# Kernel optimization log

Measured on AMD Instinct MI355X. Metric: run time of the kernel, lower is better.

Reference implementation:

```python
import jax, jax.numpy as jnp
import numpy as np


def setup_inputs() -> dict:
    key = jax.random.key(0)
    ks = jax.random.split(key, 8)
    B, IN, P, D1, D2, C = 1024, 4096, 512, 8, 16, 4
    H1, H2 = D1 * P, D2 * P
    H3 = H2 // 4
    return {
        "data_omics": jax.random.normal(ks[0], (B, IN), jnp.float32),
        "comp": jax.random.randint(ks[1], (IN, P), 0, 2, jnp.int32),
        "fc1_w": jax.random.normal(ks[2], (IN, H1), jnp.float32) * (2.0 / (IN + H1)) ** 0.5,
        "fc1_b": jax.random.uniform(ks[3], (H1,), jnp.float32),
        "fc2_w": jax.random.normal(ks[4], (H1, H2), jnp.float32) * (2.0 / (H1 + H2)) ** 0.5,
        "fc2_b": jax.random.uniform(ks[5], (H2,), jnp.float32),
        "w3": jax.random.normal(ks[6], (H2, H3), jnp.float32) * (2.0 / (H2 + H3)) ** 0.5,
        "b3": jnp.zeros((H3,), jnp.float32),
        "w4": jax.random.normal(ks[7], (H3, C), jnp.float32) * (2.0 / (H3 + C)) ** 0.5,
        "b4": jnp.zeros((C,), jnp.float32),
    }


def reference(data_omics, comp, fc1_w, fc1_b, fc2_w, fc2_b, w3, b3, w4, b4):
    P = comp.shape[1]
    D1 = fc1_w.shape[1] // P          # dim_per_path_1
    D2 = fc2_w.shape[1] // P          # dim_per_path_2
    # mask_1: [input_dim, D1*P] gene->pathway membership, repeated per hidden unit
    mask_1 = jnp.repeat(comp.astype(fc1_w.dtype), D1, axis=1)
    # mask_2: block-diagonal [D1*P, D2*P] with D1xD2 blocks of ones
    mask_2 = jnp.kron(jnp.eye(P, dtype=fc2_w.dtype), jnp.ones((D1, D2), fc2_w.dtype))
    out = jnp.matmul(data_omics, fc1_w * mask_1) + fc1_b      # [B, D1*P]
    out = jnp.matmul(out, fc2_w * mask_2) + fc2_b             # [B, D2*P]
    h = jax.nn.relu(jnp.matmul(out, w3) + b3)                 # dropout is eval no-op
    logits = jnp.matmul(h, w4) + b4                           # [B, num_classes]
    return logits
```

## Files before the change

kernel.cpp:

```cpp
#include <hip/hip_runtime.h>
#include <hip/hip_bf16.h>
#include <cstdint>
#include <cstddef>

typedef __bf16 bf16_t;
typedef __bf16 bf16x8 __attribute__((ext_vector_type(8)));
typedef float f32x4 __attribute__((ext_vector_type(4)));

#define AS1(p) ((const __attribute__((address_space(1))) void*)(p))
#define AS3(p) ((__attribute__((address_space(3))) void*)(p))

struct bf16x4_s { bf16_t x, y, z, w; };

__global__ __launch_bounds__(256) void k_transpose(const float* __restrict__ W,
                                                   const int* __restrict__ comp,
                                                   bf16_t* __restrict__ Bt,
                                                   int K, int N, int Pc) {
  __shared__ float tile[64][65];
  const int k0 = blockIdx.x * 64;
  const int n0 = blockIdx.y * 64;
  const int t = threadIdx.x;
  const int c = t & 63;
  const int r0 = t >> 6;
#pragma unroll
  for (int i = 0; i < 16; ++i) {
    int r = r0 + i * 4;
    float v = W[(size_t)(k0 + r) * N + n0 + c];
    v *= (float)comp[(size_t)(k0 + r) * Pc + ((n0 + c) >> 3)];
    tile[r][c] = v;
  }
  __syncthreads();
#pragma unroll
  for (int i = 0; i < 16; ++i) {
    int r = r0 + i * 4;
    Bt[(size_t)(n0 + r) * K + k0 + c] = (bf16_t)tile[c][r];
  }
}

__global__ __launch_bounds__(256) void k_w23(const float* __restrict__ fc2w,
                                             const float* __restrict__ w3,
                                             const float* __restrict__ b2,
                                             bf16_t* __restrict__ W23t,
                                             float* __restrict__ b23) {
  __shared__ float w3s[128][65];
  const int n0 = blockIdx.x * 64;
  const int pb = blockIdx.y * 8;
  const int tid = threadIdx.x;
  const int c = tid & 63, q = tid >> 6;
#pragma unroll
  for (int i = 0; i < 32; ++i) {
    int rr = i * 4 + q;
    w3s[rr][c] = w3[(size_t)(pb * 16 + rr) * 2048 + n0 + c];
  }
  __syncthreads();
  const int pp = c >> 3;
  const int k1 = pb * 8 + c;
  const int p = pb + pp;
  float f2[16];
  const float4* frp = (const float4*)(fc2w + (size_t)k1 * 8192 + (size_t)p * 16);
#pragma unroll
  for (int t4 = 0; t4 < 4; ++t4) {
    float4 v = frp[t4];
    f2[t4 * 4 + 0] = v.x; f2[t4 * 4 + 1] = v.y; f2[t4 * 4 + 2] = v.z; f2[t4 * 4 + 3] = v.w;
  }
#pragma unroll
  for (int i = 0; i < 16; ++i) {
    int nn = i * 4 + q;
    float s = 0.f;
#pragma unroll
    for (int d2 = 0; d2 < 16; ++d2) {
      int d2r = (d2 + 2 * pp) & 15;
      s += f2[d2r] * w3s[pp * 16 + d2r][nn];
    }
    W23t[(size_t)(n0 + nn) * 4096 + k1] = (bf16_t)s;
  }
  float bp = 0.f;
  for (int rr = q * 32; rr < q * 32 + 32; ++rr)
    bp += b2[pb * 16 + rr] * w3s[rr][c];
  atomicAdd(&b23[n0 + c], bp);
}

template<int MI, int NI, bool AF32>
__global__ __launch_bounds__(256, 2) void k_gemm_sk(const void* __restrict__ Av,
                                                    const bf16_t* __restrict__ Bt,
                                                    float* __restrict__ P,
                                                    int M, int N, int K, int ksub) {
  constexpr int BM = MI * 32;
  constexpr int BN = NI * 32;
  constexpr int BK = 32;
  __shared__ bf16_t As[BM][BK];
  __shared__ bf16_t Bs[BN][BK];
  const int tid = threadIdx.x;
  const int wave = tid >> 6;
  const int lane = tid & 63;
  const int m0 = blockIdx.y * BM;
  const int n0 = blockIdx.x * BN;
  const int kbase = blockIdx.z * ksub;
  const int wm = (wave >> 1) * (MI * 16);
  const int wn = (wave & 1) * (NI * 16);
  const int lrow = lane >> 2;
  const int lk = (lane & 3) * 8;
  const int fr = lane & 15;
  const int fkb = (lane >> 4) * 8;

  f32x4 acc[MI][NI] = {};
  const int nkt = ksub / BK;
  for (int kt = 0; kt < nkt; ++kt) {
    const int k0 = kbase + kt * BK;
    if constexpr (AF32) {
      const float* Af = (const float*)Av;
      for (int i = wave; i < BM / 16; i += 4) {
        const float* g = Af + (size_t)(m0 + i * 16 + lrow) * K + k0 + lk;
        float4 a0 = *(const float4*)g;
        float4 a1 = *(const float4*)(g + 4);
        bf16x8 v;
        v[0] = (bf16_t)a0.x; v[1] = (bf16_t)a0.y; v[2] = (bf16_t)a0.z; v[3] = (bf16_t)a0.w;
        v[4] = (bf16_t)a1.x; v[5] = (bf16_t)a1.y; v[6] = (bf16_t)a1.z; v[7] = (bf16_t)a1.w;
        *reinterpret_cast<bf16x8*>(&As[i * 16 + lrow][lk]) = v;
      }
    } else {
      const bf16_t* Ab = (const bf16_t*)Av;
      for (int i = wave; i < BM / 16; i += 4) {
        const bf16_t* g = Ab + (size_t)(m0 + i * 16 + lrow) * K + k0 + lk;
        __builtin_amdgcn_global_load_lds(AS1(g), AS3(&As[i * 16][0]), 16, 0, 0);
      }
    }
    for (int i = wave; i < BN / 16; i += 4) {
      const bf16_t* g = Bt + (size_t)(n0 + i * 16 + lrow) * K + k0 + lk;
      __builtin_amdgcn_global_load_lds(AS1(g), AS3(&Bs[i * 16][0]), 16, 0, 0);
    }
    __syncthreads();

    bf16x8 af[MI], bfr[NI];
#pragma unroll
    for (int mi = 0; mi < MI; ++mi)
      af[mi] = *reinterpret_cast<const bf16x8*>(&As[wm + mi * 16 + fr][fkb]);
#pragma unroll
    for (int ni = 0; ni < NI; ++ni)
      bfr[ni] = *reinterpret_cast<const bf16x8*>(&Bs[wn + ni * 16 + fr][fkb]);
#pragma unroll
    for (int mi = 0; mi < MI; ++mi)
#pragma unroll
      for (int ni = 0; ni < NI; ++ni)
        acc[mi][ni] = __builtin_amdgcn_mfma_f32_16x16x32_bf16(af[mi], bfr[ni], acc[mi][ni], 0, 0, 0);
    __syncthreads();
  }

  float* Po = P + (size_t)blockIdx.z * ((size_t)M * N);
  const int fq = lane >> 4;
#pragma unroll
  for (int mi = 0; mi < MI; ++mi)
#pragma unroll
    for (int ni = 0; ni < NI; ++ni) {
      const int col = n0 + wn + ni * 16 + fr;
#pragma unroll
      for (int j = 0; j < 4; ++j) {
        const int row = m0 + wm + mi * 16 + fq * 4 + j;
        Po[(size_t)row * N + col] = acc[mi][ni][j];
      }
    }
}

template<int S, bool RELU, bool B2>
__global__ __launch_bounds__(256) void k_reduce(const float* __restrict__ P, size_t sz,
                                                const float* __restrict__ bias1,
                                                const float* __restrict__ bias2,
                                                bf16_t* __restrict__ out, int N) {
  const size_t i = (size_t)blockIdx.x * 256 + threadIdx.x;
  const size_t off = i * 4;
  float4 a = *(const float4*)(P + off);
#pragma unroll
  for (int s = 1; s < S; ++s) {
    float4 t = *(const float4*)(P + (size_t)s * sz + off);
    a.x += t.x; a.y += t.y; a.z += t.z; a.w += t.w;
  }
  const int col = (int)(off & (size_t)(N - 1));
  const float4 b1 = *(const float4*)(bias1 + col);
  a.x += b1.x; a.y += b1.y; a.z += b1.z; a.w += b1.w;
  if (B2) {
    const float4 b2v = *(const float4*)(bias2 + col);
    a.x += b2v.x; a.y += b2v.y; a.z += b2v.z; a.w += b2v.w;
  }
  if (RELU) {
    a.x = fmaxf(a.x, 0.f); a.y = fmaxf(a.y, 0.f);
    a.z = fmaxf(a.z, 0.f); a.w = fmaxf(a.w, 0.f);
  }
  bf16x4_s o{(bf16_t)a.x, (bf16_t)a.y, (bf16_t)a.z, (bf16_t)a.w};
  reinterpret_cast<bf16x4_s*>(out)[i] = o;
}

__global__ __launch_bounds__(256) void k_head(const bf16_t* __restrict__ h,
                                              const float* __restrict__ W4,
                                              const float* __restrict__ b4,
                                              float* __restrict__ out) {
  const int b = blockIdx.x;
  const int n = threadIdx.x >> 6;
  const int lane = threadIdx.x & 63;
  float s = 0.f;
  for (int k = lane; k < 2048; k += 64)
    s += (float)h[(size_t)b * 2048 + k] * W4[k * 4 + n];
#pragma unroll
  for (int off = 32; off; off >>= 1) s += __shfl_down(s, off);
  if (lane == 0) out[b * 4 + n] = s + b4[n];
}

extern "C" void kernel_launch(void* const* d_in, const int* in_sizes, int n_in,
                              void* d_out, int out_size, void* d_ws, size_t ws_size,
                              hipStream_t stream) {
  const float* data  = (const float*)d_in[0];
  const int*   comp  = (const int*)d_in[1];
  const float* fc1_w = (const float*)d_in[2];
  const float* fc1_b = (const float*)d_in[3];
  const float* fc2_w = (const float*)d_in[4];
  const float* fc2_b = (const float*)d_in[5];
  const float* w3    = (const float*)d_in[6];
  const float* b3    = (const float*)d_in[7];
  const float* w4    = (const float*)d_in[8];
  const float* b4    = (const float*)d_in[9];
  float* logits = (float*)d_out;

  char* ws = (char*)d_ws;
  bf16_t* Bt1  = (bf16_t*)(ws);
  bf16_t* out1 = (bf16_t*)(ws);
  bf16_t* W23t = (bf16_t*)(ws + 8388608);
  float*  b23  = (float*)(ws + 25165824);
  bf16_t* hbuf = (bf16_t*)(ws + 25174016);
  float*  P    = (float*)(ws + 33554432);

  k_transpose<<<dim3(64, 64), 256, 0, stream>>>(fc1_w, comp, Bt1, 4096, 4096, 512);
  k_gemm_sk<4, 4, true><<<dim3(32, 8, 2), 256, 0, stream>>>(data, Bt1, P, 1024, 4096, 4096, 2048);
  k_reduce<2, false, false><<<4096, 256, 0, stream>>>(P, (size_t)1024 * 4096, fc1_b, nullptr, out1, 4096);
  hipMemsetAsync(b23, 0, 8192, stream);
  k_w23<<<dim3(32, 64), 256, 0, stream>>>(fc2_w, w3, fc2_b, W23t, b23);
  k_gemm_sk<4, 4, false><<<dim3(16, 8, 4), 256, 0, stream>>>(out1, W23t, P, 1024, 2048, 4096, 1024);
  k_reduce<4, true, true><<<2048, 256, 0, stream>>>(P, (size_t)1024 * 2048, b23, b3, hbuf, 2048);
  k_head<<<1024, 256, 0, stream>>>(hbuf, w4, b4, logits);
}
```

Measured before the change: 458.5 us.

## Triple-buffer GEMM, pre-cast input, deepen split-K, fuse reduce with head

Replaces the split-K GEMM with a triple-buffered LDS pipeline. It issues global-to-LDS loads two K-tiles ahead, uses raw waitcnt and barrier instead of two __syncthreads per tile, and raises MFMA priority. The input activations are cast to bf16 in a separate kernel so both GEMMs use the direct LDS load path. The split-K factor doubles when the workspace is large enough, which adds partial-buffer traffic but gives more blocks. The second reduction is fused with the ReLU and the 4-class head via atomics, removing the hidden-buffer round trip and one kernel, at the cost of non-deterministic summation order.

```diff
diff --git a/kernel.cpp b/kernel.cpp
--- a/kernel.cpp
+++ b/kernel.cpp
@@ -11,6 +11,16 @@
 #define AS3(p) ((__attribute__((address_space(3))) void*)(p))
 
 struct bf16x4_s { bf16_t x, y, z, w; };
+
+__global__ __launch_bounds__(256) void k_cast_bf16(const float4* __restrict__ in,
+                                                   bf16x4_s* __restrict__ out, int n4) {
+  int i = blockIdx.x * 256 + threadIdx.x;
+  if (i < n4) {
+    float4 v = in[i];
+    bf16x4_s o{(bf16_t)v.x, (bf16_t)v.y, (bf16_t)v.z, (bf16_t)v.w};
+    out[i] = o;
+  }
+}
 
 __global__ __launch_bounds__(256) void k_transpose(const float* __restrict__ W,
                                                    const int* __restrict__ comp,
@@ -80,78 +90,74 @@
   atomicAdd(&b23[n0 + c], bp);
 }
 
-template<int MI, int NI, bool AF32>
-__global__ __launch_bounds__(256, 2) void k_gemm_sk(const void* __restrict__ Av,
-                                                    const bf16_t* __restrict__ Bt,
-                                                    float* __restrict__ P,
-                                                    int M, int N, int K, int ksub) {
-  constexpr int BM = MI * 32;
-  constexpr int BN = NI * 32;
-  constexpr int BK = 32;
-  __shared__ bf16_t As[BM][BK];
-  __shared__ bf16_t Bs[BN][BK];
-  const int tid = threadIdx.x;
-  const int wave = tid >> 6;
-  const int lane = tid & 63;
-  const int m0 = blockIdx.y * BM;
-  const int n0 = blockIdx.x * BN;
+__global__ __launch_bounds__(256, 3)
+void k_gemm3(const bf16_t* __restrict__ A,
+             const bf16_t* __restrict__ Bt,
+             float* __restrict__ P,
+             int M, int N, int K, int ksub) {
+  __shared__ bf16_t lds[3][2][4096];
+  const int tid = threadIdx.x, wave = tid >> 6, lane = tid & 63;
+  const int m0 = blockIdx.y * 128, n0 = blockIdx.x * 128;
   const int kbase = blockIdx.z * ksub;
-  const int wm = (wave >> 1) * (MI * 16);
-  const int wn = (wave & 1) * (NI * 16);
-  const int lrow = lane >> 2;
-  const int lk = (lane & 3) * 8;
+  const int sfr = lane & 15;
+  const int skc = lane >> 4;
   const int fr = lane & 15;
-  const int fkb = (lane >> 4) * 8;
-
-  f32x4 acc[MI][NI] = {};
-  const int nkt = ksub / BK;
-  for (int kt = 0; kt < nkt; ++kt) {
-    const int k0 = kbase + kt * BK;
-    if constexpr (AF32) {
-      const float* Af = (const float*)Av;
-      for (int i = wave; i < BM / 16; i += 4) {
-        const float* g = Af + (size_t)(m0 + i * 16 + lrow) * K + k0 + lk;
-        float4 a0 = *(const float4*)g;
-        float4 a1 = *(const float4*)(g + 4);
-        bf16x8 v;
-        v[0] = (bf16_t)a0.x; v[1] = (bf16_t)a0.y; v[2] = (bf16_t)a0.z; v[3] = (bf16_t)a0.w;
-        v[4] = (bf16_t)a1.x; v[5] = (bf16_t)a1.y; v[6] = (bf16_t)a1.z; v[7] = (bf16_t)a1.w;
-        *reinterpret_cast<bf16x8*>(&As[i * 16 + lrow][lk]) = v;
-      }
+  const int wm16 = (wave >> 1) * 4;
+  const int wn16 = (wave & 1) * 4;
+  const int wm = wm16 * 16, wn = wn16 * 16;
+
+  const int nkt = ksub / 32;
+
+  auto stage = [&](int kt, int b) {
+    const int k0 = kbase + kt * 32 + skc * 8;
+#pragma unroll
+    for (int s = 0; s < 2; ++s) {
+      const int gi = wave + s * 4;
+      const bf16_t* ga = A + (size_t)(m0 + gi * 16 + sfr) * K + k0;
+      __builtin_amdgcn_global_load_lds(AS1(ga), AS3(&lds[b][0][gi * 512]), 16, 0, 0);
+      const bf16_t* gb = Bt + (size_t)(n0 + gi * 16 + sfr) * K + k0;
+      __builtin_amdgcn_global_load_lds(AS1(gb), AS3(&lds[b][1][gi * 512]), 16, 0, 0);
+    }
+  };
+
+  f32x4 acc[4][4] = {};
+
+  stage(0, 0);
+  stage(1, 1);
+
+  for (int t = 0; t < nkt; ++t) {
+    if (t + 1 < nkt) {
+      asm volatile("s_waitcnt vmcnt(4)" ::: "memory");
     } else {
-      const bf16_t* Ab = (const bf16_t*)Av;
-      for (int i = wave; i < BM / 16; i += 4) {
-        const bf16_t* g = Ab + (size_t)(m0 + i * 16 + lrow) * K + k0 + lk;
-        __builtin_amdgcn_global_load_lds(AS1(g), AS3(&As[i * 16][0]), 16, 0, 0);
-      }
-    }
-    for (int i = wave; i < BN / 16; i += 4) {
-      const bf16_t* g = Bt + (size_t)(n0 + i * 16 + lrow) * K + k0 + lk;
-      __builtin_amdgcn_global_load_lds(AS1(g), AS3(&Bs[i * 16][0]), 16, 0, 0);
-    }
-    __syncthreads();
-
-    bf16x8 af[MI], bfr[NI];
-#pragma unroll
-    for (int mi = 0; mi < MI; ++mi)
-      af[mi] = *reinterpret_cast<const bf16x8*>(&As[wm + mi * 16 + fr][fkb]);
-#pragma unroll
-    for (int ni = 0; ni < NI; ++ni)
-      bfr[ni] = *reinterpret_cast<const bf16x8*>(&Bs[wn + ni * 16 + fr][fkb]);
-#pragma unroll
-    for (int mi = 0; mi < MI; ++mi)
-#pragma unroll
-      for (int ni = 0; ni < NI; ++ni)
-        acc[mi][ni] = __builtin_amdgcn_mfma_f32_16x16x32_bf16(af[mi], bfr[ni], acc[mi][ni], 0, 0, 0);
-    __syncthreads();
+      asm volatile("s_waitcnt vmcnt(0)" ::: "memory");
+    }
+    __builtin_amdgcn_s_barrier();
+    __builtin_amdgcn_sched_barrier(0);
+    if (t + 2 < nkt) stage(t + 2, (t + 2) % 3);
+
+    const int b = t % 3;
+    bf16x8 af[4], bf[4];
+#pragma unroll
+    for (int mi = 0; mi < 4; ++mi)
+      af[mi] = *reinterpret_cast<const bf16x8*>(&lds[b][0][(wm16 + mi) * 512 + lane * 8]);
+#pragma unroll
+    for (int ni = 0; ni < 4; ++ni)
+      bf[ni] = *reinterpret_cast<const bf16x8*>(&lds[b][1][(wn16 + ni) * 512 + lane * 8]);
+    __builtin_amdgcn_s_setprio(1);
+#pragma unroll
+    for (int mi = 0; mi < 4; ++mi)
+#pragma unroll
+      for (int ni = 0; ni < 4; ++ni)
+        acc[mi][ni] = __builtin_amdgcn_mfma_f32_16x16x32_bf16(af[mi], bf[ni], acc[mi][ni], 0, 0, 0);
+    __builtin_amdgcn_s_setprio(0);
   }
 
   float* Po = P + (size_t)blockIdx.z * ((size_t)M * N);
   const int fq = lane >> 4;
 #pragma unroll
-  for (int mi = 0; mi < MI; ++mi)
-#pragma unroll
-    for (int ni = 0; ni < NI; ++ni) {
+  for (int mi = 0; mi < 4; ++mi)
+#pragma unroll
+    for (int ni = 0; ni < 4; ++ni) {
       const int col = n0 + wn + ni * 16 + fr;
 #pragma unroll
       for (int j = 0; j < 4; ++j) {
@@ -161,10 +167,9 @@
     }
 }
 
-template<int S, bool RELU, bool B2>
+template<int S>
 __global__ __launch_bounds__(256) void k_reduce(const float* __restrict__ P, size_t sz,
                                                 const float* __restrict__ bias1,
-                                                const float* __restrict__ bias2,
                                                 bf16_t* __restrict__ out, int N) {
   const size_t i = (size_t)blockIdx.x * 256 + threadIdx.x;
   const size_t off = i * 4;
@@ -177,31 +182,59 @@
   const int col = (int)(off & (size_t)(N - 1));
   const float4 b1 = *(const float4*)(bias1 + col);
   a.x += b1.x; a.y += b1.y; a.z += b1.z; a.w += b1.w;
-  if (B2) {
-    const float4 b2v = *(const float4*)(bias2 + col);
-    a.x += b2v.x; a.y += b2v.y; a.z += b2v.z; a.w += b2v.w;
-  }
-  if (RELU) {
-    a.x = fmaxf(a.x, 0.f); a.y = fmaxf(a.y, 0.f);
-    a.z = fmaxf(a.z, 0.f); a.w = fmaxf(a.w, 0.f);
-  }
   bf16x4_s o{(bf16_t)a.x, (bf16_t)a.y, (bf16_t)a.z, (bf16_t)a.w};
   reinterpret_cast<bf16x4_s*>(out)[i] = o;
 }
 
-__global__ __launch_bounds__(256) void k_head(const bf16_t* __restrict__ h,
-                                              const float* __restrict__ W4,
-                                              const float* __restrict__ b4,
-                                              float* __restrict__ out) {
-  const int b = blockIdx.x;
-  const int n = threadIdx.x >> 6;
-  const int lane = threadIdx.x & 63;
-  float s = 0.f;
-  for (int k = lane; k < 2048; k += 64)
-    s += (float)h[(size_t)b * 2048 + k] * W4[k * 4 + n];
-#pragma unroll
-  for (int off = 32; off; off >>= 1) s += __shfl_down(s, off);
-  if (lane == 0) out[b * 4 + n] = s + b4[n];
+__global__ __launch_bounds__(256) void k_init_logits(const float* __restrict__ b4,
+                                                     float* __restrict__ logits) {
+  int i = blockIdx.x * 256 + threadIdx.x;
+  if (i < 4096) logits[i] = b4[i & 3];
+}
+
+template<int S>
+__global__ __launch_bounds__(256) void k_reduce2_head(const float* __restrict__ P, size_t sz,
+                                                      const float* __restrict__ b23,
+                                                      const float* __restrict__ b3,
+                                                      const float* __restrict__ w4,
+                                                      float* __restrict__ logits) {
+  const int bi = blockIdx.x >> 1;
+  const int half = blockIdx.x & 1;
+  const int col = half * 1024 + threadIdx.x * 4;
+  const size_t off = (size_t)bi * 2048 + col;
+  float4 a = *(const float4*)(P + off);
+#pragma unroll
+  for (int s = 1; s < S; ++s) {
+    float4 t = *(const float4*)(P + (size_t)s * sz + off);
+    a.x += t.x; a.y += t.y; a.z += t.z; a.w += t.w;
+  }
+  const float4 bb1 = *(const float4*)(b23 + col);
+  const float4 bb2 = *(const float4*)(b3 + col);
+  float h[4];
+  h[0] = fmaxf(a.x + bb1.x + bb2.x, 0.f);
+  h[1] = fmaxf(a.y + bb1.y + bb2.y, 0.f);
+  h[2] = fmaxf(a.z + bb1.z + bb2.z, 0.f);
+  h[3] = fmaxf(a.w + bb1.w + bb2.w, 0.f);
+  float s4[4] = {0.f, 0.f, 0.f, 0.f};
+#pragma unroll
+  for (int j = 0; j < 4; ++j) {
+    const float4 w = *(const float4*)(w4 + (size_t)(col + j) * 4);
+    s4[0] += h[j] * w.x; s4[1] += h[j] * w.y; s4[2] += h[j] * w.z; s4[3] += h[j] * w.w;
+  }
+  __shared__ float red[4][4];
+  const int wave = threadIdx.x >> 6, lane = threadIdx.x & 63;
+#pragma unroll
+  for (int c = 0; c < 4; ++c) {
+    float v = s4[c];
+#pragma unroll
+    for (int o = 32; o; o >>= 1) v += __shfl_down(v, o);
+    if (lane == 0) red[wave][c] = v;
+  }
+  __syncthreads();
+  if (threadIdx.x < 4) {
+    float v = red[0][threadIdx.x] + red[1][threadIdx.x] + red[2][threadIdx.x] + red[3][threadIdx.x];
+    atomicAdd(&logits[bi * 4 + threadIdx.x], v);
+  }
 }
 
 extern "C" void kernel_launch(void* const* d_in, const int* in_sizes, int n_in,
@@ -220,19 +253,27 @@
   float* logits = (float*)d_out;
 
   char* ws = (char*)d_ws;
-  bf16_t* Bt1  = (bf16_t*)(ws);
-  bf16_t* out1 = (bf16_t*)(ws);
-  bf16_t* W23t = (bf16_t*)(ws + 8388608);
-  float*  b23  = (float*)(ws + 25165824);
-  bf16_t* hbuf = (bf16_t*)(ws + 25174016);
-  float*  P    = (float*)(ws + 33554432);
-
+  const size_t MB = 1024 * 1024;
+  const bool big = ws_size >= 104 * MB;
+  const int z1 = big ? 4 : 2;
+  const int z2 = big ? 8 : 4;
+
+  bf16_t* dataB = (bf16_t*)(ws);
+  bf16_t* Bt1   = (bf16_t*)(ws + 8 * MB);
+  float*  P     = (float*)(ws + 40 * MB);
+  bf16_t* out1  = (bf16_t*)(ws);
+  bf16_t* W23t  = (bf16_t*)(ws + 8 * MB);
+  float*  b23   = (float*)(ws + 24 * MB);
+
+  k_cast_bf16<<<4096, 256, 0, stream>>>((const float4*)data, (bf16x4_s*)dataB, 1048576);
   k_transpose<<<dim3(64, 64), 256, 0, stream>>>(fc1_w, comp, Bt1, 4096, 4096, 512);
-  k_gemm_sk<4, 4, true><<<dim3(32, 8, 2), 256, 0, stream>>>(data, Bt1, P, 1024, 4096, 4096, 2048);
-  k_reduce<2, false, false><<<4096, 256, 0, stream>>>(P, (size_t)1024 * 4096, fc1_b, nullptr, out1, 4096);
+  k_gemm3<<<dim3(32, 8, z1), 256, 0, stream>>>(dataB, Bt1, P, 1024, 4096, 4096, 4096 / z1);
+  if (big) k_reduce<4><<<4096, 256, 0, stream>>>(P, (size_t)1024 * 4096, fc1_b, out1, 4096);
+  else     k_reduce<2><<<4096, 256, 0, stream>>>(P, (size_t)1024 * 4096, fc1_b, out1, 4096);
   hipMemsetAsync(b23, 0, 8192, stream);
   k_w23<<<dim3(32, 64), 256, 0, stream>>>(fc2_w, w3, fc2_b, W23t, b23);
-  k_gemm_sk<4, 4, false><<<dim3(16, 8, 4), 256, 0, stream>>>(out1, W23t, P, 1024, 2048, 4096, 1024);
-  k_reduce<4, true, true><<<2048, 256, 0, stream>>>(P, (size_t)1024 * 2048, b23, b3, hbuf, 2048);
-  k_head<<<1024, 256, 0, stream>>>(hbuf, w4, b4, logits);
-}
+  k_gemm3<<<dim3(16, 8, z2), 256, 0, stream>>>(out1, W23t, P, 1024, 2048, 4096, 4096 / z2);
+  k_init_logits<<<16, 256, 0, stream>>>(b4, logits);
+  if (big) k_reduce2_head<8><<<2048, 256, 0, stream>>>(P, (size_t)1024 * 2048, b23, b3, w4, logits);
+  else     k_reduce2_head<4><<<2048, 256, 0, stream>>>(P, (size_t)1024 * 2048, b23, b3, w4, logits);
+}
```

Measured after the change: 415.8 us. 9.3% less time.
